# Kernel tuning notes

Hardware: AMD Instinct MI355X
Metric: run time of the kernel (lower is better)

## Reference

```python
import jax, jax.numpy as jnp
import numpy as np

B, L, D = 8, 4096, 256
H, C = 2, 128
DEG = 16  # incoming ring neighbors per node (excluding self loop)


def _build_edge_index():
    # Block-diagonal graph replicated per batch element, like _get_buffer.
    i = np.arange(L)
    offs = np.arange(1, DEG + 1)
    src_g = ((i[:, None] + offs[None, :]) % L).reshape(-1)   # [L*DEG]
    dst_g = np.repeat(i, DEG)                                 # [L*DEG]
    base = (np.arange(B) * L)[:, None]
    src = (src_g[None, :] + base).reshape(-1)
    dst = (dst_g[None, :] + base).reshape(-1)
    # PyG GATConv: remove_self_loops + add_self_loops -> exactly one self loop/node
    self_idx = np.arange(B * L)
    src = np.concatenate([src, self_idx])
    dst = np.concatenate([dst, self_idx])
    return jnp.asarray(np.stack([src, dst]), dtype=jnp.int32)  # [2, E]


def setup_inputs() -> dict:
    key = jax.random.key(0)
    k0, k1, k2, k3 = jax.random.split(key, 4)
    glorot = 1.0 / np.sqrt(D)
    return {
        "x": jax.random.normal(k0, (B, L, D), jnp.float32),
        "edge_index": _build_edge_index(),
        "W": jax.random.normal(k1, (D, H * C), jnp.float32) * glorot,
        "att_src": jax.random.normal(k2, (H, C), jnp.float32) * (1.0 / np.sqrt(C)),
        "att_dst": jax.random.normal(k3, (H, C), jnp.float32) * (1.0 / np.sqrt(C)),
        "bias": jnp.zeros((H * C,), jnp.float32),
    }


def reference(x, edge_index, W, att_src, att_dst, bias):
    b, l, d = x.shape
    n = b * l
    h_, c_ = att_src.shape
    xf = x.reshape(n, d)                                   # flatten batch of graphs
    res = xf
    h = (xf @ W).reshape(n, h_, c_)                        # [N,H,C] projected features
    a_src = jnp.einsum('nhc,hc->nh', h, att_src)           # per-node src logits
    a_dst = jnp.einsum('nhc,hc->nh', h, att_dst)
    s, t = edge_index[0], edge_index[1]
    alpha = jax.nn.leaky_relu(a_src[s] + a_dst[t], 0.2)    # [E,H]
    # softmax over incoming edges of each destination node
    amax = jax.ops.segment_max(alpha, t, num_segments=n)
    ex = jnp.exp(alpha - amax[t])
    denom = jax.ops.segment_sum(ex, t, num_segments=n)
    attn = ex / jnp.where(denom[t] > 0, denom[t], 1.0)     # [E,H]
    msg = h[s] * attn[:, :, None]                          # [E,H,C]
    out = jax.ops.segment_sum(msg, t, num_segments=n).reshape(n, h_ * c_) + bias
    out = jax.nn.relu(out) + res                           # relu + residual
    return out.reshape(b, l, h_ * c_)
```

## Files before the change

### kernel.cpp

```cpp
#include <hip/hip_runtime.h>

#define LL 4096
#define DD 256
#define TM 32
#define HALO 16
#define ROWS (TM + HALO)
#define NTH 256
#define APAD 40
#define HTS 56
#define WBS 40
#define ABUF_BYTES (ROWS * APAD * 2)

typedef float f32x4 __attribute__((ext_vector_type(4)));
typedef __bf16 bf16x8 __attribute__((ext_vector_type(8)));
typedef unsigned short us8 __attribute__((ext_vector_type(8)));
typedef unsigned short us4 __attribute__((ext_vector_type(4)));
typedef unsigned int u32x2 __attribute__((ext_vector_type(2)));

__device__ __forceinline__ unsigned short f2bf(float f) {
    union { float f; unsigned u; } v; v.f = f;
    unsigned r = v.u + 0x7fffu + ((v.u >> 16) & 1u);
    return (unsigned short)(r >> 16);
}

__device__ __forceinline__ unsigned cvtpk_bf16(float a, float b) {
    unsigned r;
    asm("v_cvt_pk_bf16_f32 %0, %1, %2" : "=v"(r) : "v"(a), "v"(b));
    return r;
}

#define KBAR() do {                                         \
    asm volatile("s_waitcnt lgkmcnt(0)" ::: "memory");      \
    __builtin_amdgcn_s_barrier();                           \
} while (0)

__global__ void prep_w(const float* __restrict__ W, unsigned short* __restrict__ Wt) {
    __shared__ unsigned short wl[32][260];
    const int tid = threadIdx.x;
    const int kk = blockIdx.x;
    for (int lin = tid; lin < 2048; lin += 512) {
        int r = lin >> 6;
        int q = lin & 63;
        const float4 v = *reinterpret_cast<const float4*>(W + (kk * 32 + r) * 256 + q * 4);
        us4 p;
        p[0] = f2bf(v.x); p[1] = f2bf(v.y); p[2] = f2bf(v.z); p[3] = f2bf(v.w);
        *reinterpret_cast<us4*>(&wl[r][q * 4]) = p;
    }
    __syncthreads();
    for (int id = tid; id < 1024; id += 512) {
        int ct = id >> 6, l = id & 63;
        int lo = l & 15, hi = l >> 4;
        us8 v;
        for (int j = 0; j < 8; ++j) v[j] = wl[hi * 8 + j][ct * 16 + lo];
        *reinterpret_cast<us8*>(Wt + (size_t)(((ct * 8 + kk) * 64 + l) * 8)) = v;
    }
}

__global__ __launch_bounds__(NTH, 4) void gat_fused(
    const float* __restrict__ x, const unsigned short* __restrict__ Wt,
    const float* __restrict__ att_src, const float* __restrict__ att_dst,
    const float* __restrict__ bias, float* __restrict__ out)
{
    __shared__ unsigned short h_t[256][HTS];
    __shared__ float alog[ROWS][2][2];
    __shared__ __align__(16) unsigned char smem_u[2 * ABUF_BYTES];
    unsigned short (*abuf0)[APAD] = reinterpret_cast<unsigned short(*)[APAD]>(smem_u);
    unsigned short (*abuf1)[APAD] = reinterpret_cast<unsigned short(*)[APAD]>(smem_u + ABUF_BYTES);
    unsigned short (*wband)[WBS]  = reinterpret_cast<unsigned short(*)[WBS]>(smem_u);

    const int tid  = threadIdx.x;
    const int lane = tid & 63;
    const int wv   = tid >> 6;
    const int lo   = lane & 15;
    const int hi   = lane >> 4;
    const int blk  = blockIdx.x;
    const int batch = blk >> 7;
    const int i0    = (blk & 127) * TM;
    const long xbase = (long)batch * (LL * DD);
    const int ct0 = wv * 4;
    const int hd  = wv >> 1;

    if (tid < 192) ((float*)alog)[tid] = 0.f;

    f32x4 acc[3][4];
    for (int a = 0; a < 3; ++a)
        for (int b = 0; b < 4; ++b)
            acc[a][b] = (f32x4){0.f, 0.f, 0.f, 0.f};

    const int s0r = tid >> 3, s0k = (tid & 7) << 2;
    const int s1r = (tid + 256) >> 3, s1k = (tid & 7) << 2;
    const float* xrow0 = x + xbase + (long)((i0 + s0r) & (LL - 1)) * DD + s0k;
    const float* xrow1 = x + xbase + (long)((i0 + s1r) & (LL - 1)) * DD + s1k;
    const unsigned short* wtb0 = Wt + (size_t)((ct0 + 0) * 8 * 64 + lane) * 8;
    const unsigned short* wtb1 = Wt + (size_t)((ct0 + 1) * 8 * 64 + lane) * 8;
    const unsigned short* wtb2 = Wt + (size_t)((ct0 + 2) * 8 * 64 + lane) * 8;
    const unsigned short* wtb3 = Wt + (size_t)((ct0 + 3) * 8 * 64 + lane) * 8;

    float4 cur0, cur1, nxt0, nxt1;
    us8 braw0, braw1, braw2, braw3;

    cur0 = *reinterpret_cast<const float4*>(xrow0);
    if (tid < 128) cur1 = *reinterpret_cast<const float4*>(xrow1);
    braw0 = *reinterpret_cast<const us8*>(wtb0);
    braw1 = *reinterpret_cast<const us8*>(wtb1);
    braw2 = *reinterpret_cast<const us8*>(wtb2);
    braw3 = *reinterpret_cast<const us8*>(wtb3);
    {
        u32x2 p;
        p[0] = cvtpk_bf16(cur0.x, cur0.y);
        p[1] = cvtpk_bf16(cur0.z, cur0.w);
        *reinterpret_cast<u32x2*>(&abuf0[s0r][s0k]) = p;
        if (tid < 128) {
            u32x2 q;
            q[0] = cvtpk_bf16(cur1.x, cur1.y);
            q[1] = cvtpk_bf16(cur1.z, cur1.w);
            *reinterpret_cast<u32x2*>(&abuf0[s1r][s1k]) = q;
        }
    }

#pragma unroll
    for (int kk = 0; kk < 8; ++kk) {
        unsigned short (*buf)[APAD]  = (kk & 1) ? abuf1 : abuf0;
        unsigned short (*nbuf)[APAD] = (kk & 1) ? abuf0 : abuf1;
        if (kk < 7) {
            nxt0 = *reinterpret_cast<const float4*>(xrow0 + (kk + 1) * 32);
            if (tid < 128) nxt1 = *reinterpret_cast<const float4*>(xrow1 + (kk + 1) * 32);
        }
        KBAR();

        bf16x8 bf0 = __builtin_bit_cast(bf16x8, braw0);
        bf16x8 bf1 = __builtin_bit_cast(bf16x8, braw1);
        bf16x8 bf2 = __builtin_bit_cast(bf16x8, braw2);
        bf16x8 bf3 = __builtin_bit_cast(bf16x8, braw3);
        for (int rt = 0; rt < 3; ++rt) {
            us8 araw = *reinterpret_cast<const us8*>(&buf[rt * 16 + lo][hi * 8]);
            bf16x8 afrag = __builtin_bit_cast(bf16x8, araw);
            acc[rt][0] = __builtin_amdgcn_mfma_f32_16x16x32_bf16(bf0, afrag, acc[rt][0], 0, 0, 0);
            acc[rt][1] = __builtin_amdgcn_mfma_f32_16x16x32_bf16(bf1, afrag, acc[rt][1], 0, 0, 0);
            acc[rt][2] = __builtin_amdgcn_mfma_f32_16x16x32_bf16(bf2, afrag, acc[rt][2], 0, 0, 0);
            acc[rt][3] = __builtin_amdgcn_mfma_f32_16x16x32_bf16(bf3, afrag, acc[rt][3], 0, 0, 0);
        }

        if (kk < 7) {
            braw0 = *reinterpret_cast<const us8*>(wtb0 + (size_t)(kk + 1) * 512);
            braw1 = *reinterpret_cast<const us8*>(wtb1 + (size_t)(kk + 1) * 512);
            braw2 = *reinterpret_cast<const us8*>(wtb2 + (size_t)(kk + 1) * 512);
            braw3 = *reinterpret_cast<const us8*>(wtb3 + (size_t)(kk + 1) * 512);
            u32x2 p;
            p[0] = cvtpk_bf16(nxt0.x, nxt0.y);
            p[1] = cvtpk_bf16(nxt0.z, nxt0.w);
            *reinterpret_cast<u32x2*>(&nbuf[s0r][s0k]) = p;
            if (tid < 128) {
                u32x2 q;
                q[0] = cvtpk_bf16(nxt1.x, nxt1.y);
                q[1] = cvtpk_bf16(nxt1.z, nxt1.w);
                *reinterpret_cast<u32x2*>(&nbuf[s1r][s1k]) = q;
            }
        }
    }

    {
        float4 as[4], ad[4];
#pragma unroll
        for (int c = 0; c < 4; ++c) {
            as[c] = *reinterpret_cast<const float4*>(att_src + (ct0 + c) * 16 + hi * 4);
            ad[c] = *reinterpret_cast<const float4*>(att_dst + (ct0 + c) * 16 + hi * 4);
        }
        float ps[3], pd[3];
        for (int rt = 0; rt < 3; ++rt) {
            ps[rt] = 0.f; pd[rt] = 0.f;
            int xrow = rt * 16 + lo;
#pragma unroll
            for (int c = 0; c < 4; ++c) {
                f32x4 a = acc[rt][c];
                ps[rt] += a[0] * as[c].x + a[1] * as[c].y + a[2] * as[c].z + a[3] * as[c].w;
                pd[rt] += a[0] * ad[c].x + a[1] * ad[c].y + a[2] * ad[c].z + a[3] * ad[c].w;
                unsigned pk0 = cvtpk_bf16(a[0], a[1]);
                unsigned pk1 = cvtpk_bf16(a[2], a[3]);
                int chan = (ct0 + c) * 16 + hi * 4;
                h_t[chan + 0][xrow] = (unsigned short)pk0;
                h_t[chan + 1][xrow] = (unsigned short)(pk0 >> 16);
                h_t[chan + 2][xrow] = (unsigned short)pk1;
                h_t[chan + 3][xrow] = (unsigned short)(pk1 >> 16);
            }
        }
        for (int rt = 0; rt < 3; ++rt) {
            ps[rt] += __shfl_xor(ps[rt], 16);
            ps[rt] += __shfl_xor(ps[rt], 32);
            pd[rt] += __shfl_xor(pd[rt], 16);
            pd[rt] += __shfl_xor(pd[rt], 32);
        }
        if (hi == 0) {
            for (int rt = 0; rt < 3; ++rt) {
                atomicAdd(&alog[rt * 16 + lo][hd][0], ps[rt]);
                atomicAdd(&alog[rt * 16 + lo][hd][1], pd[rt]);
            }
        }
    }

    float4 res[2][4];
    for (int ti = 0; ti < 2; ++ti)
#pragma unroll
        for (int c = 0; c < 4; ++c)
            res[ti][c] = *reinterpret_cast<const float4*>(
                x + xbase + (long)(i0 + ti * 16 + lo) * DD + (ct0 + c) * 16 + hi * 4);

    __syncthreads();

    if (tid < 64) {
        int r = tid >> 1, h2 = tid & 1;
        unsigned short* wrow = &wband[h2 * 32 + r][0];
        us8 z = {0, 0, 0, 0, 0, 0, 0, 0};
        for (int q = 0; q < 5; ++q) *reinterpret_cast<us8*>(wrow + q * 8) = z;
        float ad = alog[r][h2][1];
        float al[17];
        float mx = -1e30f;
        for (int k = 0; k < 17; ++k) {
            float s = (k < 16) ? alog[r + 1 + k][h2][0] : alog[r][h2][0];
            float v = s + ad;
            v = (v > 0.f) ? v : 0.2f * v;
            al[k] = v;
            mx = fmaxf(mx, v);
        }
        float sum = 0.f;
        for (int k = 0; k < 17; ++k) { al[k] = __expf(al[k] - mx); sum += al[k]; }
        float inv = 1.f / sum;
        int lo_r = r & 15;
        wrow[lo_r] = f2bf(al[16] * inv);
        for (int k = 0; k < 16; ++k) wrow[lo_r + 1 + k] = f2bf(al[k] * inv);
    }
    __syncthreads();

    {
        f32x4 acc2[2][4];
        for (int a = 0; a < 2; ++a)
            for (int b = 0; b < 4; ++b)
                acc2[a][b] = (f32x4){0.f, 0.f, 0.f, 0.f};

        for (int ti = 0; ti < 2; ++ti) {
            us8 raw = *reinterpret_cast<const us8*>(&wband[hd * 32 + ti * 16 + lo][hi * 8]);
            bf16x8 bfr = __builtin_bit_cast(bf16x8, raw);
#pragma unroll
            for (int c = 0; c < 4; ++c) {
                us8 araw = *reinterpret_cast<const us8*>(
                    &h_t[(ct0 + c) * 16 + lo][ti * 16 + hi * 8]);
                bf16x8 afr = __builtin_bit_cast(bf16x8, araw);
                acc2[ti][c] = __builtin_amdgcn_mfma_f32_16x16x32_bf16(afr, bfr, acc2[ti][c], 0, 0, 0);
            }
        }

        for (int ti = 0; ti < 2; ++ti)
#pragma unroll
            for (int c = 0; c < 4; ++c) {
                const float4 b4 = *reinterpret_cast<const float4*>(bias + (ct0 + c) * 16 + hi * 4);
                f32x4 s = acc2[ti][c];
                long g = xbase + (long)(i0 + ti * 16 + lo) * DD + (ct0 + c) * 16 + hi * 4;
                float4 o;
                o.x = fmaxf(s[0] + b4.x, 0.f) + res[ti][c].x;
                o.y = fmaxf(s[1] + b4.y, 0.f) + res[ti][c].y;
                o.z = fmaxf(s[2] + b4.z, 0.f) + res[ti][c].z;
                o.w = fmaxf(s[3] + b4.w, 0.f) + res[ti][c].w;
                *reinterpret_cast<float4*>(out + g) = o;
            }
    }
}

extern "C" void kernel_launch(void* const* d_in, const int* in_sizes, int n_in,
                              void* d_out, int out_size, void* d_ws, size_t ws_size,
                              hipStream_t stream) {
    const float* x       = (const float*)d_in[0];
    const float* W       = (const float*)d_in[2];
    const float* att_src = (const float*)d_in[3];
    const float* att_dst = (const float*)d_in[4];
    const float* bias    = (const float*)d_in[5];
    float* out           = (float*)d_out;
    unsigned short* Wt   = (unsigned short*)d_ws;

    hipLaunchKernelGGL(prep_w, dim3(8), dim3(512), 0, stream, W, Wt);
    hipLaunchKernelGGL(gat_fused, dim3(1024), dim3(NTH), 0, stream,
                       x, Wt, att_src, att_dst, bias, out);
}
```

Before: 30.50 us.

## Stage full fp32 x tile into LDS via async global_load_lds, drop per-k barriers

The double-buffered pipeline loaded, converted and stored bf16 A-tiles with a barrier on every k step. The new code instead DMAs the whole 48-row fp32 x tile into LDS up front with global_load_lds, using an XOR swizzle, behind a single barrier. Each k step then reads fp32 fragments from LDS and packs them to bf16 in registers, while the W fragments are prefetched one step ahead. h_t and wband now alias the same 48KB buffer, and h_t is written after a barrier. This removes the per-step synchronisation, but the larger LDS footprint may reduce blocks per CU.

```diff
diff --git a/kernel.cpp b/kernel.cpp
--- a/kernel.cpp
+++ b/kernel.cpp
@@ -6,16 +6,14 @@
 #define HALO 16
 #define ROWS (TM + HALO)
 #define NTH 256
-#define APAD 40
 #define HTS 56
 #define WBS 40
-#define ABUF_BYTES (ROWS * APAD * 2)
 
 typedef float f32x4 __attribute__((ext_vector_type(4)));
 typedef __bf16 bf16x8 __attribute__((ext_vector_type(8)));
 typedef unsigned short us8 __attribute__((ext_vector_type(8)));
 typedef unsigned short us4 __attribute__((ext_vector_type(4)));
-typedef unsigned int u32x2 __attribute__((ext_vector_type(2)));
+typedef unsigned int u32x4 __attribute__((ext_vector_type(4)));
 
 __device__ __forceinline__ unsigned short f2bf(float f) {
     union { float f; unsigned u; } v; v.f = f;
@@ -61,12 +59,11 @@
     const float* __restrict__ att_src, const float* __restrict__ att_dst,
     const float* __restrict__ bias, float* __restrict__ out)
 {
-    __shared__ unsigned short h_t[256][HTS];
+    __shared__ __align__(16) unsigned char smem_u[ROWS * DD * 4];
+    float* xf32 = (float*)smem_u;
+    unsigned short (*h_t)[HTS]  = (unsigned short(*)[HTS])smem_u;
+    unsigned short (*wband)[WBS] = (unsigned short(*)[WBS])(smem_u + 256 * HTS * 2);
     __shared__ float alog[ROWS][2][2];
-    __shared__ __align__(16) unsigned char smem_u[2 * ABUF_BYTES];
-    unsigned short (*abuf0)[APAD] = reinterpret_cast<unsigned short(*)[APAD]>(smem_u);
-    unsigned short (*abuf1)[APAD] = reinterpret_cast<unsigned short(*)[APAD]>(smem_u + ABUF_BYTES);
-    unsigned short (*wband)[WBS]  = reinterpret_cast<unsigned short(*)[WBS]>(smem_u);
 
     const int tid  = threadIdx.x;
     const int lane = tid & 63;
@@ -82,81 +79,64 @@
 
     if (tid < 192) ((float*)alog)[tid] = 0.f;
 
+#pragma unroll
+    for (int i = 0; i < 12; ++i) {
+        int row = wv * 12 + i;
+        const float* gp = x + xbase + (long)((i0 + row) & (LL - 1)) * DD
+                        + ((lane ^ (row & 7)) << 2);
+        __builtin_amdgcn_global_load_lds(
+            (__attribute__((address_space(1))) const void*)gp,
+            (__attribute__((address_space(3))) void*)(xf32 + row * DD),
+            16, 0, 0);
+    }
+
+    const unsigned short* wtb0 = Wt + (size_t)((ct0 + 0) * 8 * 64 + lane) * 8;
+    const unsigned short* wtb1 = Wt + (size_t)((ct0 + 1) * 8 * 64 + lane) * 8;
+    const unsigned short* wtb2 = Wt + (size_t)((ct0 + 2) * 8 * 64 + lane) * 8;
+    const unsigned short* wtb3 = Wt + (size_t)((ct0 + 3) * 8 * 64 + lane) * 8;
+    us8 braw0 = *reinterpret_cast<const us8*>(wtb0);
+    us8 braw1 = *reinterpret_cast<const us8*>(wtb1);
+    us8 braw2 = *reinterpret_cast<const us8*>(wtb2);
+    us8 braw3 = *reinterpret_cast<const us8*>(wtb3);
+
+    __syncthreads();
+
     f32x4 acc[3][4];
     for (int a = 0; a < 3; ++a)
         for (int b = 0; b < 4; ++b)
             acc[a][b] = (f32x4){0.f, 0.f, 0.f, 0.f};
 
-    const int s0r = tid >> 3, s0k = (tid & 7) << 2;
-    const int s1r = (tid + 256) >> 3, s1k = (tid & 7) << 2;
-    const float* xrow0 = x + xbase + (long)((i0 + s0r) & (LL - 1)) * DD + s0k;
-    const float* xrow1 = x + xbase + (long)((i0 + s1r) & (LL - 1)) * DD + s1k;
-    const unsigned short* wtb0 = Wt + (size_t)((ct0 + 0) * 8 * 64 + lane) * 8;
-    const unsigned short* wtb1 = Wt + (size_t)((ct0 + 1) * 8 * 64 + lane) * 8;
-    const unsigned short* wtb2 = Wt + (size_t)((ct0 + 2) * 8 * 64 + lane) * 8;
-    const unsigned short* wtb3 = Wt + (size_t)((ct0 + 3) * 8 * 64 + lane) * 8;
-
-    float4 cur0, cur1, nxt0, nxt1;
-    us8 braw0, braw1, braw2, braw3;
-
-    cur0 = *reinterpret_cast<const float4*>(xrow0);
-    if (tid < 128) cur1 = *reinterpret_cast<const float4*>(xrow1);
-    braw0 = *reinterpret_cast<const us8*>(wtb0);
-    braw1 = *reinterpret_cast<const us8*>(wtb1);
-    braw2 = *reinterpret_cast<const us8*>(wtb2);
-    braw3 = *reinterpret_cast<const us8*>(wtb3);
-    {
-        u32x2 p;
-        p[0] = cvtpk_bf16(cur0.x, cur0.y);
-        p[1] = cvtpk_bf16(cur0.z, cur0.w);
-        *reinterpret_cast<u32x2*>(&abuf0[s0r][s0k]) = p;
-        if (tid < 128) {
-            u32x2 q;
-            q[0] = cvtpk_bf16(cur1.x, cur1.y);
-            q[1] = cvtpk_bf16(cur1.z, cur1.w);
-            *reinterpret_cast<u32x2*>(&abuf0[s1r][s1k]) = q;
-        }
-    }
-
+    const int s7 = lo & 7;
+    us8 nbraw0, nbraw1, nbraw2, nbraw3;
 #pragma unroll
     for (int kk = 0; kk < 8; ++kk) {
-        unsigned short (*buf)[APAD]  = (kk & 1) ? abuf1 : abuf0;
-        unsigned short (*nbuf)[APAD] = (kk & 1) ? abuf0 : abuf1;
         if (kk < 7) {
-            nxt0 = *reinterpret_cast<const float4*>(xrow0 + (kk + 1) * 32);
-            if (tid < 128) nxt1 = *reinterpret_cast<const float4*>(xrow1 + (kk + 1) * 32);
-        }
-        KBAR();
-
+            nbraw0 = *reinterpret_cast<const us8*>(wtb0 + (size_t)(kk + 1) * 512);
+            nbraw1 = *reinterpret_cast<const us8*>(wtb1 + (size_t)(kk + 1) * 512);
+            nbraw2 = *reinterpret_cast<const us8*>(wtb2 + (size_t)(kk + 1) * 512);
+            nbraw3 = *reinterpret_cast<const us8*>(wtb3 + (size_t)(kk + 1) * 512);
+        }
         bf16x8 bf0 = __builtin_bit_cast(bf16x8, braw0);
         bf16x8 bf1 = __builtin_bit_cast(bf16x8, braw1);
         bf16x8 bf2 = __builtin_bit_cast(bf16x8, braw2);
         bf16x8 bf3 = __builtin_bit_cast(bf16x8, braw3);
         for (int rt = 0; rt < 3; ++rt) {
-            us8 araw = *reinterpret_cast<const us8*>(&buf[rt * 16 + lo][hi * 8]);
-            bf16x8 afrag = __builtin_bit_cast(bf16x8, araw);
+            int row = rt * 16 + lo;
+            int g0 = kk * 8 + hi * 2;
+            f32x4 a0 = *reinterpret_cast<const f32x4*>(&xf32[row * DD + (((g0    ) ^ s7) << 2)]);
+            f32x4 a1 = *reinterpret_cast<const f32x4*>(&xf32[row * DD + (((g0 + 1) ^ s7) << 2)]);
+            u32x4 q;
+            q[0] = cvtpk_bf16(a0[0], a0[1]);
+            q[1] = cvtpk_bf16(a0[2], a0[3]);
+            q[2] = cvtpk_bf16(a1[0], a1[1]);
+            q[3] = cvtpk_bf16(a1[2], a1[3]);
+            bf16x8 afrag = __builtin_bit_cast(bf16x8, q);
             acc[rt][0] = __builtin_amdgcn_mfma_f32_16x16x32_bf16(bf0, afrag, acc[rt][0], 0, 0, 0);
             acc[rt][1] = __builtin_amdgcn_mfma_f32_16x16x32_bf16(bf1, afrag, acc[rt][1], 0, 0, 0);
             acc[rt][2] = __builtin_amdgcn_mfma_f32_16x16x32_bf16(bf2, afrag, acc[rt][2], 0, 0, 0);
             acc[rt][3] = __builtin_amdgcn_mfma_f32_16x16x32_bf16(bf3, afrag, acc[rt][3], 0, 0, 0);
         }
-
-        if (kk < 7) {
-            braw0 = *reinterpret_cast<const us8*>(wtb0 + (size_t)(kk + 1) * 512);
-            braw1 = *reinterpret_cast<const us8*>(wtb1 + (size_t)(kk + 1) * 512);
-            braw2 = *reinterpret_cast<const us8*>(wtb2 + (size_t)(kk + 1) * 512);
-            braw3 = *reinterpret_cast<const us8*>(wtb3 + (size_t)(kk + 1) * 512);
-            u32x2 p;
-            p[0] = cvtpk_bf16(nxt0.x, nxt0.y);
-            p[1] = cvtpk_bf16(nxt0.z, nxt0.w);
-            *reinterpret_cast<u32x2*>(&nbuf[s0r][s0k]) = p;
-            if (tid < 128) {
-                u32x2 q;
-                q[0] = cvtpk_bf16(nxt1.x, nxt1.y);
-                q[1] = cvtpk_bf16(nxt1.z, nxt1.w);
-                *reinterpret_cast<u32x2*>(&nbuf[s1r][s1k]) = q;
-            }
-        }
+        if (kk < 7) { braw0 = nbraw0; braw1 = nbraw1; braw2 = nbraw2; braw3 = nbraw3; }
     }
 
     {
@@ -169,19 +149,11 @@
         float ps[3], pd[3];
         for (int rt = 0; rt < 3; ++rt) {
             ps[rt] = 0.f; pd[rt] = 0.f;
-            int xrow = rt * 16 + lo;
 #pragma unroll
             for (int c = 0; c < 4; ++c) {
                 f32x4 a = acc[rt][c];
                 ps[rt] += a[0] * as[c].x + a[1] * as[c].y + a[2] * as[c].z + a[3] * as[c].w;
                 pd[rt] += a[0] * ad[c].x + a[1] * ad[c].y + a[2] * ad[c].z + a[3] * ad[c].w;
-                unsigned pk0 = cvtpk_bf16(a[0], a[1]);
-                unsigned pk1 = cvtpk_bf16(a[2], a[3]);
-                int chan = (ct0 + c) * 16 + hi * 4;
-                h_t[chan + 0][xrow] = (unsigned short)pk0;
-                h_t[chan + 1][xrow] = (unsigned short)(pk0 >> 16);
-                h_t[chan + 2][xrow] = (unsigned short)pk1;
-                h_t[chan + 3][xrow] = (unsigned short)(pk1 >> 16);
             }
         }
         for (int rt = 0; rt < 3; ++rt) {
@@ -198,14 +170,29 @@
         }
     }
 
+    KBAR();
+
+    for (int rt = 0; rt < 3; ++rt) {
+        int xrow = rt * 16 + lo;
+#pragma unroll
+        for (int c = 0; c < 4; ++c) {
+            f32x4 a = acc[rt][c];
+            unsigned pk0 = cvtpk_bf16(a[0], a[1]);
+            unsigned pk1 = cvtpk_bf16(a[2], a[3]);
+            int chan = (ct0 + c) * 16 + hi * 4;
+            h_t[chan + 0][xrow] = (unsigned short)pk0;
+            h_t[chan + 1][xrow] = (unsigned short)(pk0 >> 16);
+            h_t[chan + 2][xrow] = (unsigned short)pk1;
+            h_t[chan + 3][xrow] = (unsigned short)(pk1 >> 16);
+        }
+    }
+
     float4 res[2][4];
     for (int ti = 0; ti < 2; ++ti)
 #pragma unroll
         for (int c = 0; c < 4; ++c)
             res[ti][c] = *reinterpret_cast<const float4*>(
                 x + xbase + (long)(i0 + ti * 16 + lo) * DD + (ct0 + c) * 16 + hi * 4);
-
-    __syncthreads();
 
     if (tid < 64) {
         int r = tid >> 1, h2 = tid & 1;
@@ -229,7 +216,8 @@
         wrow[lo_r] = f2bf(al[16] * inv);
         for (int k = 0; k < 16; ++k) wrow[lo_r + 1 + k] = f2bf(al[k] * inv);
     }
-    __syncthreads();
+
+    KBAR();
 
     {
         f32x4 acc2[2][4];
```

New measurement: 38.59 us. +26.6%, slower.
